# Kernel tuning notes

Hardware: AMD Instinct MI355X
Metric: run time of the kernel (lower is better)

The kernel has to match this reference:

```python
import jax, jax.numpy as jnp
import numpy as np


def _sage_layer(x, neighbors, W, b):
    # x: (N, D), neighbors: (N, deg) int indices into x
    neigh_agg = x[neighbors].mean(axis=1)           # (N, D) gather + mean
    h = jnp.concatenate([x, neigh_agg], axis=-1)     # (N, 2D)
    return jax.nn.relu(h @ W + b)                    # (N, D_out)


def setup_inputs() -> dict:
    key = jax.random.key(0)
    k1, k2, k3, k4 = jax.random.split(key, 4)
    N, D, DEG = 50000, 128, 16
    x = jax.random.normal(k1, (N, D), dtype=jnp.float32)
    neighbors = jax.random.randint(k2, (N, DEG), 0, N)
    # Linear(in_dim*2, out_dim) weights, stored as (2D, D_out) for x @ W
    scale = 1.0 / np.sqrt(2 * D)
    W1 = jax.random.normal(k3, (2 * D, D), dtype=jnp.float32) * scale
    b1 = jnp.zeros((D,), dtype=jnp.float32)
    W2 = jax.random.normal(k4, (2 * D, D), dtype=jnp.float32) * scale
    b2 = jnp.zeros((D,), dtype=jnp.float32)
    return {"x": x, "neighbors": neighbors, "W1": W1, "b1": b1, "W2": W2, "b2": b2}


def reference(x, neighbors, W1, b1, W2, b2):
    h = _sage_layer(x, neighbors, W1, b1)
    h = _sage_layer(h, neighbors, W2, b2)
    return h
```

## Files before the change

### kernel.cpp

```cpp
#include <hip/hip_runtime.h>

typedef __attribute__((ext_vector_type(8))) short short8;
typedef __attribute__((ext_vector_type(4))) float f32x4;
typedef __attribute__((ext_vector_type(2))) float f32x2;

#define N_NODES 50000
#define D 128
#define DEG 16
#define BM 32

static __device__ __forceinline__ unsigned short f2b(float f) {
    union { float f; unsigned int u; } v; v.f = f;
    return (unsigned short)((v.u + 0x7fffu + ((v.u >> 16) & 1u)) >> 16);
}

__global__ void prep(const float* __restrict__ x, unsigned short* __restrict__ xb,
                     unsigned char* __restrict__ xq,
                     const float* __restrict__ W1, const float* __restrict__ W2,
                     unsigned short* __restrict__ Wf1, unsigned short* __restrict__ Wf2) {
    int b = blockIdx.x;
    if (b < 32) {
        int o  = (b * 256 + threadIdx.x) * 4;
        int e0 = o & 7;
        int l  = (o >> 3) & 63;
        int ct = (o >> 9) & 1;
        int kk = (o >> 10) & 7;
        int w  = o >> 13;
        int n  = w * 32 + ((l & 15) << 1) + ct;
        int kb = kk * 32 + (l >> 4) * 8 + e0;
        ushort4 a, c;
        a.x = f2b(W1[(kb + 0) * D + n]);
        a.y = f2b(W1[(kb + 1) * D + n]);
        a.z = f2b(W1[(kb + 2) * D + n]);
        a.w = f2b(W1[(kb + 3) * D + n]);
        *(ushort4*)(Wf1 + o) = a;
        c.x = f2b(W2[(kb + 0) * D + n]);
        c.y = f2b(W2[(kb + 1) * D + n]);
        c.z = f2b(W2[(kb + 2) * D + n]);
        c.w = f2b(W2[(kb + 3) * D + n]);
        *(ushort4*)(Wf2 + o) = c;
    } else {
        int i = ((b - 32) * 256 + threadIdx.x) * 4;
        if (i < N_NODES * D) {
            float4 v = *(const float4*)(x + i);
            ushort4 o4;
            o4.x = f2b(v.x); o4.y = f2b(v.y); o4.z = f2b(v.z); o4.w = f2b(v.w);
            *(ushort4*)(xb + i) = o4;
            int q = __builtin_amdgcn_cvt_pk_fp8_f32(v.x, v.y, 0, false);
            q = __builtin_amdgcn_cvt_pk_fp8_f32(v.z, v.w, q, true);
            *(unsigned*)(xq + i) = (unsigned)q;
        }
    }
}

template <int OUT_BF16>
__global__ __launch_bounds__(256, 4)
void sage_layer(const unsigned short* __restrict__ feat,
                const unsigned char* __restrict__ featq,
                const int* __restrict__ nbr,
                const unsigned short* __restrict__ wf,
                const float* __restrict__ bias,
                void* __restrict__ out,
                unsigned char* __restrict__ outq)
{
    __shared__ __align__(16) unsigned short Hl[BM * 264];
    __shared__ int Nl[BM * DEG];
    const int tid  = threadIdx.x;
    const int row0 = blockIdx.x * BM;

    if (tid < 128) {
        int g = row0 * DEG + tid * 4;
        int gmax = N_NODES * DEG - 4;
        if (g > gmax) g = gmax;
        *(int4*)(Nl + tid * 4) = *(const int4*)(nbr + g);
    }
    __syncthreads();

    const char* fb = (const char*)feat;
    const char* qb = (const char*)featq;

    #pragma unroll
    for (int p = 0; p < 2; ++p) {
        int a = tid + p * 256;
        int r = a >> 4;
        int s = a & 15;
        int grow = row0 + r;
        if (grow >= N_NODES) grow = N_NODES - 1;
        short8 self = *(const short8*)(fb + (unsigned)grow * 256u + (unsigned)s * 16u);

        int4 i0 = *(const int4*)(Nl + r * 16);
        int4 i1 = *(const int4*)(Nl + r * 16 + 4);
        int4 i2 = *(const int4*)(Nl + r * 16 + 8);
        int4 i3 = *(const int4*)(Nl + r * 16 + 12);
        int ids[16] = { i0.x, i0.y, i0.z, i0.w, i1.x, i1.y, i1.z, i1.w,
                        i2.x, i2.y, i2.z, i2.w, i3.x, i3.y, i3.z, i3.w };

        uint2 v[16];
        #pragma unroll
        for (int j = 0; j < 16; ++j)
            v[j] = *(const uint2*)(qb + (((unsigned)ids[j]) << 7) + (unsigned)s * 8u);

        f32x2 am[4];
        #pragma unroll
        for (int i = 0; i < 4; ++i) am[i] = (f32x2){0.f, 0.f};
        #pragma unroll
        for (int j = 0; j < 16; ++j) {
            am[0] += __builtin_amdgcn_cvt_pk_f32_fp8(v[j].x, false);
            am[1] += __builtin_amdgcn_cvt_pk_f32_fp8(v[j].x, true);
            am[2] += __builtin_amdgcn_cvt_pk_f32_fp8(v[j].y, false);
            am[3] += __builtin_amdgcn_cvt_pk_f32_fp8(v[j].y, true);
        }

        unsigned short* hr = Hl + r * 264 + s * 8;
        *(short8*)(hr) = self;
        union { unsigned short u[8]; short8 s8; } m;
        #pragma unroll
        for (int i = 0; i < 4; ++i) {
            m.u[2 * i]     = f2b(am[i].x * 0.0625f);
            m.u[2 * i + 1] = f2b(am[i].y * 0.0625f);
        }
        *(short8*)(hr + D) = m.s8;
    }

    const int lane = tid & 63;
    const int w    = tid >> 6;
    const int quad = lane >> 4;
    const int l16  = lane & 15;
    const unsigned short* wfw = wf + w * 8192;
    short8 bfrag[8][2];
    #pragma unroll
    for (int kk = 0; kk < 8; ++kk)
        #pragma unroll
        for (int ct = 0; ct < 2; ++ct)
            bfrag[kk][ct] = *(const short8*)(wfw + kk * 1024 + ct * 512 + lane * 8);

    __syncthreads();

    f32x4 acc[2][2];
    #pragma unroll
    for (int rt = 0; rt < 2; ++rt)
        #pragma unroll
        for (int ct = 0; ct < 2; ++ct)
            acc[rt][ct] = (f32x4){0.f, 0.f, 0.f, 0.f};

    #pragma unroll
    for (int kk = 0; kk < 8; ++kk) {
        short8 af[2];
        #pragma unroll
        for (int rt = 0; rt < 2; ++rt)
            af[rt] = *(const short8*)(&Hl[(rt * 16 + l16) * 264 + kk * 32 + quad * 8]);
        #pragma unroll
        for (int rt = 0; rt < 2; ++rt)
            #pragma unroll
            for (int ct = 0; ct < 2; ++ct)
                acc[rt][ct] = __builtin_amdgcn_mfma_f32_16x16x32_bf16(
                    af[rt], bfrag[kk][ct], acc[rt][ct], 0, 0, 0);
    }

    const int col0 = w * 32 + (l16 << 1);
    float2 bv = *(const float2*)(bias + col0);
    #pragma unroll
    for (int rt = 0; rt < 2; ++rt) {
        int gb = row0 + rt * 16 + quad * 4;
        #pragma unroll
        for (int r = 0; r < 4; ++r) {
            int grow = gb + r;
            if (grow >= N_NODES) continue;
            float v0 = acc[rt][0][r] + bv.x;
            float v1 = acc[rt][1][r] + bv.y;
            v0 = v0 > 0.f ? v0 : 0.f;
            v1 = v1 > 0.f ? v1 : 0.f;
            if (OUT_BF16) {
                unsigned u = (unsigned)f2b(v0) | ((unsigned)f2b(v1) << 16);
                *(unsigned*)((unsigned short*)out + grow * D + col0) = u;
                int q = __builtin_amdgcn_cvt_pk_fp8_f32(v0, v1, 0, false);
                *(unsigned short*)(outq + grow * D + col0) = (unsigned short)q;
            } else {
                f32x2 o2; o2.x = v0; o2.y = v1;
                *(f32x2*)((float*)out + grow * D + col0) = o2;
            }
        }
    }
}

extern "C" void kernel_launch(void* const* d_in, const int* in_sizes, int n_in,
                              void* d_out, int out_size, void* d_ws, size_t ws_size,
                              hipStream_t stream) {
    const float* x  = (const float*)d_in[0];
    const int*   nb = (const int*)d_in[1];
    const float* W1 = (const float*)d_in[2];
    const float* b1 = (const float*)d_in[3];
    const float* W2 = (const float*)d_in[4];
    const float* b2 = (const float*)d_in[5];

    char* ws = (char*)d_ws;
    unsigned short* Wf1 = (unsigned short*)(ws);
    unsigned short* Wf2 = (unsigned short*)(ws + 65536);
    unsigned short* xb  = (unsigned short*)(ws + 131072);
    unsigned short* h1  = (unsigned short*)(ws + 131072 + 12800000);
    unsigned char*  xq  = (unsigned char*)(ws + 131072 + 25600000);
    unsigned char*  h1q = (unsigned char*)(ws + 131072 + 32000000);

    prep<<<32 + 6250, 256, 0, stream>>>(x, xb, xq, W1, W2, Wf1, Wf2);

    const int mgrid = (N_NODES + BM - 1) / BM;
    sage_layer<1><<<mgrid, 256, 0, stream>>>(xb, xq, nb, Wf1, b1, h1, h1q);
    sage_layer<0><<<mgrid, 256, 0, stream>>>(h1, h1q, nb, Wf2, b2, d_out, nullptr);
}
```

Before: 124.9 us.

## Fuse prep and both SAGE layers into one persistent kernel with grid barriers

Replaces the three launches (prep, layer 1, layer 2) with a single persistent kernel of 1024 blocks. The blocks loop over prep units and row tiles and meet at software grid barriers built on atomic counters, which a memset clears before each launch. The aim is to remove launch gaps and tail effects between stages. It depends on all 1024 blocks being resident at once (256 threads, launch bounds allowing 4 per CU), adds barrier spin cost, and adds an extra memset per call. The prep loop also now handles 8 elements per thread instead of 4.

```diff
diff --git a/kernel.cpp b/kernel.cpp
--- a/kernel.cpp
+++ b/kernel.cpp
@@ -8,19 +8,35 @@
 #define D 128
 #define DEG 16
 #define BM 32
+#define GRID 1024
+#define NTILES 1563
+#define PREP_UNITS 3157
 
 static __device__ __forceinline__ unsigned short f2b(float f) {
     union { float f; unsigned int u; } v; v.f = f;
     return (unsigned short)((v.u + 0x7fffu + ((v.u >> 16) & 1u)) >> 16);
 }
 
-__global__ void prep(const float* __restrict__ x, unsigned short* __restrict__ xb,
-                     unsigned char* __restrict__ xq,
-                     const float* __restrict__ W1, const float* __restrict__ W2,
-                     unsigned short* __restrict__ Wf1, unsigned short* __restrict__ Wf2) {
-    int b = blockIdx.x;
-    if (b < 32) {
-        int o  = (b * 256 + threadIdx.x) * 4;
+static __device__ __forceinline__ void gridbar(unsigned* cnt) {
+    __syncthreads();
+    if (threadIdx.x == 0) {
+        __threadfence();
+        __hip_atomic_fetch_add(cnt, 1u, __ATOMIC_RELEASE, __HIP_MEMORY_SCOPE_AGENT);
+        while (__hip_atomic_load(cnt, __ATOMIC_RELAXED, __HIP_MEMORY_SCOPE_AGENT) < GRID)
+            __builtin_amdgcn_s_sleep(8);
+        __threadfence();
+    }
+    __syncthreads();
+}
+
+static __device__ __forceinline__ void prep_unit(
+    int u, int tid, const float* __restrict__ x,
+    const float* __restrict__ W1, const float* __restrict__ W2,
+    unsigned short* __restrict__ xb, unsigned char* __restrict__ xq,
+    unsigned short* __restrict__ Wf1, unsigned short* __restrict__ Wf2)
+{
+    if (u < 32) {
+        int o  = (u * 256 + tid) * 4;
         int e0 = o & 7;
         int l  = (o >> 3) & 63;
         int ct = (o >> 9) & 1;
@@ -40,34 +56,34 @@
         c.w = f2b(W2[(kb + 3) * D + n]);
         *(ushort4*)(Wf2 + o) = c;
     } else {
-        int i = ((b - 32) * 256 + threadIdx.x) * 4;
-        if (i < N_NODES * D) {
-            float4 v = *(const float4*)(x + i);
-            ushort4 o4;
-            o4.x = f2b(v.x); o4.y = f2b(v.y); o4.z = f2b(v.z); o4.w = f2b(v.w);
-            *(ushort4*)(xb + i) = o4;
-            int q = __builtin_amdgcn_cvt_pk_fp8_f32(v.x, v.y, 0, false);
-            q = __builtin_amdgcn_cvt_pk_fp8_f32(v.z, v.w, q, true);
-            *(unsigned*)(xq + i) = (unsigned)q;
-        }
+        int i = (u - 32) * 2048 + tid * 8;
+        float4 v0 = *(const float4*)(x + i);
+        float4 v1 = *(const float4*)(x + i + 4);
+        union { unsigned short u[8]; short8 s8; } m;
+        m.u[0] = f2b(v0.x); m.u[1] = f2b(v0.y); m.u[2] = f2b(v0.z); m.u[3] = f2b(v0.w);
+        m.u[4] = f2b(v1.x); m.u[5] = f2b(v1.y); m.u[6] = f2b(v1.z); m.u[7] = f2b(v1.w);
+        *(short8*)(xb + i) = m.s8;
+        int q0 = __builtin_amdgcn_cvt_pk_fp8_f32(v0.x, v0.y, 0, false);
+        q0 = __builtin_amdgcn_cvt_pk_fp8_f32(v0.z, v0.w, q0, true);
+        int q1 = __builtin_amdgcn_cvt_pk_fp8_f32(v1.x, v1.y, 0, false);
+        q1 = __builtin_amdgcn_cvt_pk_fp8_f32(v1.z, v1.w, q1, true);
+        uint2 qq; qq.x = (unsigned)q0; qq.y = (unsigned)q1;
+        *(uint2*)(xq + i) = qq;
     }
 }
 
 template <int OUT_BF16>
-__global__ __launch_bounds__(256, 4)
-void sage_layer(const unsigned short* __restrict__ feat,
-                const unsigned char* __restrict__ featq,
-                const int* __restrict__ nbr,
-                const unsigned short* __restrict__ wf,
-                const float* __restrict__ bias,
-                void* __restrict__ out,
-                unsigned char* __restrict__ outq)
+static __device__ __forceinline__ void layer_tile(
+    int t, const unsigned short* __restrict__ feat,
+    const unsigned char* __restrict__ featq,
+    const int* __restrict__ nbr, const unsigned short* __restrict__ wf,
+    const float* __restrict__ bias, void* __restrict__ out,
+    unsigned char* __restrict__ outq, unsigned short* Hl, int* Nl)
 {
-    __shared__ __align__(16) unsigned short Hl[BM * 264];
-    __shared__ int Nl[BM * DEG];
     const int tid  = threadIdx.x;
-    const int row0 = blockIdx.x * BM;
-
+    const int row0 = t * BM;
+
+    __syncthreads();
     if (tid < 128) {
         int g = row0 * DEG + tid * 4;
         int gmax = N_NODES * DEG - 4;
@@ -183,6 +199,34 @@
     }
 }
 
+__global__ __launch_bounds__(256, 4)
+void fused(const float* __restrict__ x, const int* __restrict__ nbr,
+           const float* __restrict__ W1, const float* __restrict__ b1,
+           const float* __restrict__ W2, const float* __restrict__ b2,
+           unsigned short* __restrict__ xb, unsigned char* __restrict__ xq,
+           unsigned short* __restrict__ h1, unsigned char* __restrict__ h1q,
+           unsigned short* __restrict__ Wf1, unsigned short* __restrict__ Wf2,
+           float* __restrict__ out, unsigned* __restrict__ cnt)
+{
+    __shared__ __align__(16) unsigned short Hl[BM * 264];
+    __shared__ __align__(16) int Nl[BM * DEG];
+    const int bid = blockIdx.x;
+    const int tid = threadIdx.x;
+
+    for (int u = bid; u < PREP_UNITS; u += GRID)
+        prep_unit(u, tid, x, W1, W2, xb, xq, Wf1, Wf2);
+
+    gridbar(cnt + 0);
+
+    for (int t = bid; t < NTILES; t += GRID)
+        layer_tile<1>(t, xb, xq, nbr, Wf1, b1, (void*)h1, h1q, Hl, Nl);
+
+    gridbar(cnt + 32);
+
+    for (int t = bid; t < NTILES; t += GRID)
+        layer_tile<0>(t, h1, h1q, nbr, Wf2, b2, (void*)out, nullptr, Hl, Nl);
+}
+
 extern "C" void kernel_launch(void* const* d_in, const int* in_sizes, int n_in,
                               void* d_out, int out_size, void* d_ws, size_t ws_size,
                               hipStream_t stream) {
@@ -200,10 +244,11 @@
     unsigned short* h1  = (unsigned short*)(ws + 131072 + 12800000);
     unsigned char*  xq  = (unsigned char*)(ws + 131072 + 25600000);
     unsigned char*  h1q = (unsigned char*)(ws + 131072 + 32000000);
-
-    prep<<<32 + 6250, 256, 0, stream>>>(x, xb, xq, W1, W2, Wf1, Wf2);
-
-    const int mgrid = (N_NODES + BM - 1) / BM;
-    sage_layer<1><<<mgrid, 256, 0, stream>>>(xb, xq, nb, Wf1, b1, h1, h1q);
-    sage_layer<0><<<mgrid, 256, 0, stream>>>(h1, h1q, nb, Wf2, b2, d_out, nullptr);
-}
+    unsigned*       cnt = (unsigned*)(ws + 40000000);
+
+    hipMemsetAsync((void*)cnt, 0, 256, stream);
+
+    fused<<<GRID, 256, 0, stream>>>(x, nb, W1, b1, W2, b2,
+                                    xb, xq, h1, h1q, Wf1, Wf2,
+                                    (float*)d_out, cnt);
+}
```

Result: slower. 393.7 us (+215.3%).
